# Kernel optimization log

Measured on AMD Instinct MI355X. Metric: run time of the kernel, lower is better.

The kernel has to match this reference:

```python
import jax, jax.numpy as jnp
import numpy as np

B, A, S, D, OUT = 8, 16384, 2048, 512, 512
REDUCTION = "mean"  # matches init_kwargs


def setup_inputs() -> dict:
    key = jax.random.key(0)
    k1, k2, k3 = jax.random.split(key, 3)
    input_rep = jax.random.normal(k1, (B, A, D), jnp.float32)
    # sorted residue ids per protein (atoms are stored residue-by-residue)
    aa_res_ids = jnp.sort(jax.random.randint(k2, (B, A), 0, S), axis=-1).astype(jnp.int32)
    input_aa_len = jnp.full((B,), A, jnp.int32)
    input_seq_len = jnp.full((B,), S, jnp.int32)
    W = jax.random.normal(k3, (OUT, D), jnp.float32) / np.sqrt(D)
    bias = jnp.zeros((OUT,), jnp.float32)
    return {"input_rep": input_rep, "aa_res_ids": aa_res_ids,
            "input_aa_len": input_aa_len, "input_seq_len": input_seq_len,
            "W": W, "bias": bias}


def _pool(input_rep, aa_res_ids, input_aa_len, input_seq_len):
    # input_rep: [B, A, D]; aa_res_ids: [B, A] in [0, S)
    Bv, Av, Dv = input_rep.shape
    valid = jnp.arange(Av)[None, :] < input_aa_len[:, None]          # [B, A] atoms within aa_len
    seg = jnp.arange(Bv)[:, None] * S + aa_res_ids                   # flatten (b, res_id) -> segment id
    seg = jnp.where(valid, seg, Bv * S)                              # invalid atoms -> dummy segment
    nseg = Bv * S + 1
    seg_f = seg.reshape(-1)
    counts = jax.ops.segment_sum(valid.reshape(-1).astype(input_rep.dtype), seg_f,
                                 num_segments=nseg)[: Bv * S].reshape(Bv, S)
    if REDUCTION == "mean":
        sums = jax.ops.segment_sum(input_rep.reshape(Bv * Av, Dv), seg_f,
                                   num_segments=nseg)[: Bv * S].reshape(Bv, S, Dv)
        pooled = sums / jnp.maximum(counts, 1)[..., None]
    elif REDUCTION == "max":
        vals = jnp.where(valid[..., None], input_rep, -jnp.inf).reshape(Bv * Av, Dv)
        pooled = jax.ops.segment_max(vals, seg_f, num_segments=nseg)[: Bv * S].reshape(Bv, S, Dv)
        pooled = jnp.where((counts > 0)[..., None], pooled, 0.0)
    else:
        raise ValueError("Unsupported reduction method: {}".format(REDUCTION))
    in_seq = jnp.arange(S)[None, :] < input_seq_len[:, None]         # [B, S] positions within seq_len
    filled = (counts > 0) & in_seq                                   # residues that received >=1 atom
    n_fill = filled.sum(axis=1)                                      # [B]
    avg = (pooled * filled[..., None]).sum(axis=1) / jnp.maximum(n_fill, 1)[:, None].astype(input_rep.dtype)
    # unfilled-but-in-range positions get the per-protein average of filled residues; out-of-range stay 0
    out = jnp.where(filled[..., None], pooled,
                    jnp.where(in_seq[..., None], avg[:, None, :], jnp.zeros((), input_rep.dtype)))
    return out


def reference(input_rep, aa_res_ids, input_aa_len, input_seq_len, W, bias):
    out = _pool(input_rep, aa_res_ids, input_aa_len, input_seq_len)  # [B, S, D]
    return out @ W.T + bias                                          # [B, S, OUT]
```

## Files before the change

kernel.cpp:

```cpp
#include <hip/hip_runtime.h>
#include <cstdint>
#include <cstddef>

#define Bv 8
#define Av 16384
#define Sv 2048
#define Dv 512
#define OUTv 512
#define Mv (Bv * Sv)

using u16 = unsigned short;
using f32x4 = __attribute__((ext_vector_type(4))) float;
using bf16x8 = __attribute__((ext_vector_type(8))) short;

__device__ __forceinline__ u16 f2bf(float x) {
  union { float f; uint32_t u; } v; v.f = x;
  uint32_t u = v.u;
  uint32_t r = u + 0x7FFFu + ((u >> 16) & 1u);
  return (u16)(r >> 16);
}
__device__ __forceinline__ float bf2f(u16 h) {
  union { uint32_t u; float f; } v; v.u = ((uint32_t)h) << 16; return v.f;
}

__device__ __forceinline__ void gl_lds16(const void* g, void* s) {
  __builtin_amdgcn_global_load_lds(
      (const __attribute__((address_space(1))) unsigned int*)g,
      (__attribute__((address_space(3))) unsigned int*)s, 16, 0, 0);
}

__global__ __launch_bounds__(128)
void pool_kernel(const float* __restrict__ rep, const int* __restrict__ res_ids,
                 const int* __restrict__ aa_len, u16* __restrict__ pooled,
                 int* __restrict__ counts) {
  const int bs = blockIdx.x;
  const int b = bs >> 11;
  const int s = bs & (Sv - 1);
  int alen = aa_len[b];
  alen = alen < 0 ? 0 : (alen > Av ? Av : alen);
  const int* ids = res_ids + b * Av;
  int lo = 0, hi = alen;
  while (lo < hi) { int mid = (lo + hi) >> 1; if (ids[mid] < s) lo = mid + 1; else hi = mid; }
  const int start = lo;
  hi = alen;
  while (lo < hi) { int mid = (lo + hi) >> 1; if (ids[mid] <= s) lo = mid + 1; else hi = mid; }
  const int end = lo;
  const int cnt = end - start;

  const int t = threadIdx.x;
  float a0 = 0.f, a1 = 0.f, a2 = 0.f, a3 = 0.f;
  float b0 = 0.f, b1 = 0.f, b2 = 0.f, b3 = 0.f;
  const float* base = rep + (size_t)b * Av * Dv + t * 4;
  int a = start;
  for (; a + 2 <= end; a += 2) {
    float4 v = *(const float4*)(base + (size_t)a * Dv);
    float4 w = *(const float4*)(base + (size_t)(a + 1) * Dv);
    a0 += v.x; a1 += v.y; a2 += v.z; a3 += v.w;
    b0 += w.x; b1 += w.y; b2 += w.z; b3 += w.w;
  }
  if (a < end) {
    float4 v = *(const float4*)(base + (size_t)a * Dv);
    a0 += v.x; a1 += v.y; a2 += v.z; a3 += v.w;
  }
  a0 += b0; a1 += b1; a2 += b2; a3 += b3;
  const float inv = cnt > 0 ? 1.0f / (float)cnt : 0.0f;
  ushort4 o = { f2bf(a0 * inv), f2bf(a1 * inv), f2bf(a2 * inv), f2bf(a3 * inv) };
  *(ushort4*)(pooled + (size_t)bs * Dv + t * 4) = o;
  if (t == 0) counts[bs] = cnt;
}

__global__ __launch_bounds__(256)
void wconv_kernel(const float* __restrict__ W, u16* __restrict__ Wb) {
  const int i = (blockIdx.x * 256 + threadIdx.x) * 4;
  float4 v = *(const float4*)(W + i);
  ushort4 o = { f2bf(v.x), f2bf(v.y), f2bf(v.z), f2bf(v.w) };
  *(ushort4*)(Wb + i) = o;
}

__global__ __launch_bounds__(128)
void avg_kernel(const u16* __restrict__ pooled, const int* __restrict__ counts,
                const int* __restrict__ seq_len, float* __restrict__ avg_sum,
                int* __restrict__ n_fill) {
  const int b = blockIdx.x;
  const int chunk = blockIdx.y;
  const int t = threadIdx.x;
  int slen = seq_len[b];
  slen = slen < 0 ? 0 : (slen > Sv ? Sv : slen);
  const int s0 = chunk * 128;
  float a0 = 0.f, a1 = 0.f, a2 = 0.f, a3 = 0.f;
  int filled = 0;
  for (int s = s0; s < s0 + 128; ++s) {
    if (s < slen && counts[b * Sv + s] > 0) {
      ++filled;
      ushort4 v = *(const ushort4*)(pooled + ((size_t)(b * Sv + s)) * Dv + t * 4);
      a0 += bf2f(v.x); a1 += bf2f(v.y); a2 += bf2f(v.z); a3 += bf2f(v.w);
    }
  }
  atomicAdd(&avg_sum[b * Dv + t * 4 + 0], a0);
  atomicAdd(&avg_sum[b * Dv + t * 4 + 1], a1);
  atomicAdd(&avg_sum[b * Dv + t * 4 + 2], a2);
  atomicAdd(&avg_sum[b * Dv + t * 4 + 3], a3);
  if (t == 0) atomicAdd(&n_fill[b], filled);
}

__global__ __launch_bounds__(64)
void fixup_kernel(u16* __restrict__ pooled, const int* __restrict__ counts,
                  const int* __restrict__ seq_len, const float* __restrict__ avg_sum,
                  const int* __restrict__ n_fill) {
  const int bs = blockIdx.x;
  const int b = bs >> 11;
  const int s = bs & (Sv - 1);
  int slen = seq_len[b];
  slen = slen < 0 ? 0 : (slen > Sv ? Sv : slen);
  const int cnt = counts[bs];
  const int t = threadIdx.x;
  if (s >= slen) {
    if (cnt != 0) {
      ushort4 z = {0, 0, 0, 0};
      *(ushort4*)(pooled + (size_t)bs * Dv + t * 8) = z;
      *(ushort4*)(pooled + (size_t)bs * Dv + t * 8 + 4) = z;
    }
    return;
  }
  if (cnt > 0) return;
  const int nf = n_fill[b];
  const float inv = 1.0f / (float)(nf > 0 ? nf : 1);
  float4 v0 = *(const float4*)(avg_sum + b * Dv + t * 8);
  float4 v1 = *(const float4*)(avg_sum + b * Dv + t * 8 + 4);
  ushort4 o0 = { f2bf(v0.x * inv), f2bf(v0.y * inv), f2bf(v0.z * inv), f2bf(v0.w * inv) };
  ushort4 o1 = { f2bf(v1.x * inv), f2bf(v1.y * inv), f2bf(v1.z * inv), f2bf(v1.w * inv) };
  *(ushort4*)(pooled + (size_t)bs * Dv + t * 8) = o0;
  *(ushort4*)(pooled + (size_t)bs * Dv + t * 8 + 4) = o1;
}

#define BM 128
#define BN 128
#define BK 64

__global__ __launch_bounds__(256, 2)
void gemm_kernel(const u16* __restrict__ A, const u16* __restrict__ Bw,
                 const float* __restrict__ bias, float* __restrict__ out) {
  __shared__ alignas(16) u16 As[BM * BK];
  __shared__ alignas(16) u16 Bs[BN * BK];
  const int tid = threadIdx.x;
  const int m0 = blockIdx.x * BM;
  const int n0 = blockIdx.y * BN;
  const int lane = tid & 63;
  const int wave = tid >> 6;
  const int wm = (wave & 1) * 64;
  const int wn = (wave >> 1) * 64;
  const int fr = lane & 15;
  const int fq = lane >> 4;

  f32x4 acc[4][4];
#pragma unroll
  for (int i = 0; i < 4; ++i)
#pragma unroll
    for (int j = 0; j < 4; ++j) acc[i][j] = (f32x4){0.f, 0.f, 0.f, 0.f};

  const char* Ab = (const char*)A;
  const char* Bb = (const char*)Bw;

  for (int k0 = 0; k0 < Dv; k0 += BK) {
    __syncthreads();
#pragma unroll
    for (int c = 0; c < 4; ++c) {
      const int off = (c * 256 + tid) * 16;
      const int row = off >> 7;
      const int inb = off & 127;
      gl_lds16(Ab + (size_t)(m0 + row) * (Dv * 2) + k0 * 2 + inb, (char*)As + off);
      gl_lds16(Bb + (size_t)(n0 + row) * (Dv * 2) + k0 * 2 + inb, (char*)Bs + off);
    }
    __syncthreads();

#pragma unroll
    for (int ks = 0; ks < 2; ++ks) {
      bf16x8 af[4], bfv[4];
#pragma unroll
      for (int mi = 0; mi < 4; ++mi)
        af[mi] = *(const bf16x8*)(As + (wm + mi * 16 + fr) * BK + ks * 32 + fq * 8);
#pragma unroll
      for (int ni = 0; ni < 4; ++ni)
        bfv[ni] = *(const bf16x8*)(Bs + (wn + ni * 16 + fr) * BK + ks * 32 + fq * 8);
#pragma unroll
      for (int mi = 0; mi < 4; ++mi)
#pragma unroll
        for (int ni = 0; ni < 4; ++ni)
          acc[mi][ni] = __builtin_amdgcn_mfma_f32_16x16x32_bf16(bfv[ni], af[mi], acc[mi][ni], 0, 0, 0);
    }
  }

#pragma unroll
  for (int mi = 0; mi < 4; ++mi) {
    const int row = m0 + wm + mi * 16 + fr;
#pragma unroll
    for (int ni = 0; ni < 4; ++ni) {
      const int colb = n0 + wn + ni * 16 + fq * 4;
      float4 bv = *(const float4*)(bias + colb);
      f32x4 v = acc[mi][ni];
      float4 o = { v[0] + bv.x, v[1] + bv.y, v[2] + bv.z, v[3] + bv.w };
      *(float4*)(out + (size_t)row * OUTv + colb) = o;
    }
  }
}

extern "C" void kernel_launch(void* const* d_in, const int* in_sizes, int n_in,
                              void* d_out, int out_size, void* d_ws, size_t ws_size,
                              hipStream_t stream) {
  (void)in_sizes; (void)n_in; (void)out_size; (void)ws_size;
  const float* rep     = (const float*)d_in[0];
  const int*   res_ids = (const int*)d_in[1];
  const int*   aa_len  = (const int*)d_in[2];
  const int*   seq_len = (const int*)d_in[3];
  const float* W       = (const float*)d_in[4];
  const float* bias    = (const float*)d_in[5];
  float* out = (float*)d_out;

  char* ws = (char*)d_ws;
  u16*   pooled  = (u16*)ws;
  u16*   Wb      = (u16*)(ws + 16777216);
  int*   counts  = (int*)(ws + 17301504);
  float* avg_sum = (float*)(ws + 17367040);
  int*   n_fill  = (int*)(ws + 17383424);

  hipMemsetAsync(avg_sum, 0, Bv * Dv * sizeof(float) + Bv * sizeof(int), stream);

  wconv_kernel<<<(OUTv * Dv) / (256 * 4), 256, 0, stream>>>(W, Wb);
  pool_kernel<<<Mv, 128, 0, stream>>>(rep, res_ids, aa_len, pooled, counts);
  avg_kernel<<<dim3(Bv, 16), 128, 0, stream>>>(pooled, counts, seq_len, avg_sum, n_fill);
  fixup_kernel<<<Mv, 64, 0, stream>>>(pooled, counts, seq_len, avg_sum, n_fill);
  gemm_kernel<<<dim3(Mv / BM, OUTv / BN), 256, 0, stream>>>(pooled, Wb, bias, out);
}
```

Before: 446.7 us.

## Precompute residue segment offsets, widen pool unroll, split avg over more blocks

Adds a kernel that scatters per-residue start offsets from the sorted residue ids, so each pool block reads two offsets instead of running two binary searches over global memory. The pool loop is unrolled to four independent row loads with separate accumulators to expose more memory parallelism. The average kernel is split into 128 chunks of 16 residues per protein to raise occupancy, at the cost of more atomics. This adds one extra launch, and the starts kernel's zero-length and tail-fill loops run serially in single threads.

Result: faster. 429.3 us (-3.9%).

```diff
diff --git a/kernel.cpp b/kernel.cpp
--- a/kernel.cpp
+++ b/kernel.cpp
@@ -29,44 +29,65 @@
       (__attribute__((address_space(3))) unsigned int*)s, 16, 0, 0);
 }
 
+__global__ __launch_bounds__(256)
+void starts_kernel(const int* __restrict__ res_ids, const int* __restrict__ aa_len,
+                   int* __restrict__ starts) {
+  const int b = blockIdx.y;
+  const int a = blockIdx.x * 256 + threadIdx.x;
+  int alen = aa_len[b];
+  alen = alen < 0 ? 0 : (alen > Av ? Av : alen);
+  int* st = starts + b * (Sv + 1);
+  if (a >= alen) {
+    if (a == 0) {
+      for (int s = 0; s <= Sv; ++s) st[s] = 0;
+    }
+    return;
+  }
+  const int* ids = res_ids + b * Av;
+  const int id = ids[a];
+  const int p = (a == 0) ? -1 : ids[a - 1];
+  for (int s = p + 1; s <= id; ++s) st[s] = a;
+  if (a == alen - 1) {
+    for (int s = id + 1; s <= Sv; ++s) st[s] = alen;
+  }
+}
+
 __global__ __launch_bounds__(128)
-void pool_kernel(const float* __restrict__ rep, const int* __restrict__ res_ids,
-                 const int* __restrict__ aa_len, u16* __restrict__ pooled,
-                 int* __restrict__ counts) {
+void pool_kernel(const float* __restrict__ rep, const int* __restrict__ starts,
+                 u16* __restrict__ pooled) {
   const int bs = blockIdx.x;
   const int b = bs >> 11;
   const int s = bs & (Sv - 1);
-  int alen = aa_len[b];
-  alen = alen < 0 ? 0 : (alen > Av ? Av : alen);
-  const int* ids = res_ids + b * Av;
-  int lo = 0, hi = alen;
-  while (lo < hi) { int mid = (lo + hi) >> 1; if (ids[mid] < s) lo = mid + 1; else hi = mid; }
-  const int start = lo;
-  hi = alen;
-  while (lo < hi) { int mid = (lo + hi) >> 1; if (ids[mid] <= s) lo = mid + 1; else hi = mid; }
-  const int end = lo;
+  const int* st = starts + b * (Sv + 1);
+  const int start = st[s];
+  const int end = st[s + 1];
   const int cnt = end - start;
 
   const int t = threadIdx.x;
-  float a0 = 0.f, a1 = 0.f, a2 = 0.f, a3 = 0.f;
-  float b0 = 0.f, b1 = 0.f, b2 = 0.f, b3 = 0.f;
+  float p0 = 0.f, p1 = 0.f, p2 = 0.f, p3 = 0.f;
+  float q0 = 0.f, q1 = 0.f, q2 = 0.f, q3 = 0.f;
+  float r0 = 0.f, r1 = 0.f, r2 = 0.f, r3 = 0.f;
+  float w0 = 0.f, w1 = 0.f, w2 = 0.f, w3 = 0.f;
   const float* base = rep + (size_t)b * Av * Dv + t * 4;
   int a = start;
-  for (; a + 2 <= end; a += 2) {
+  for (; a + 4 <= end; a += 4) {
+    float4 v0 = *(const float4*)(base + (size_t)(a + 0) * Dv);
+    float4 v1 = *(const float4*)(base + (size_t)(a + 1) * Dv);
+    float4 v2 = *(const float4*)(base + (size_t)(a + 2) * Dv);
+    float4 v3 = *(const float4*)(base + (size_t)(a + 3) * Dv);
+    p0 += v0.x; p1 += v0.y; p2 += v0.z; p3 += v0.w;
+    q0 += v1.x; q1 += v1.y; q2 += v1.z; q3 += v1.w;
+    r0 += v2.x; r1 += v2.y; r2 += v2.z; r3 += v2.w;
+    w0 += v3.x; w1 += v3.y; w2 += v3.z; w3 += v3.w;
+  }
+  for (; a < end; ++a) {
     float4 v = *(const float4*)(base + (size_t)a * Dv);
-    float4 w = *(const float4*)(base + (size_t)(a + 1) * Dv);
-    a0 += v.x; a1 += v.y; a2 += v.z; a3 += v.w;
-    b0 += w.x; b1 += w.y; b2 += w.z; b3 += w.w;
-  }
-  if (a < end) {
-    float4 v = *(const float4*)(base + (size_t)a * Dv);
-    a0 += v.x; a1 += v.y; a2 += v.z; a3 += v.w;
-  }
-  a0 += b0; a1 += b1; a2 += b2; a3 += b3;
+    p0 += v.x; p1 += v.y; p2 += v.z; p3 += v.w;
+  }
+  p0 += q0 + r0 + w0; p1 += q1 + r1 + w1; p2 += q2 + r2 + w2; p3 += q3 + r3 + w3;
   const float inv = cnt > 0 ? 1.0f / (float)cnt : 0.0f;
-  ushort4 o = { f2bf(a0 * inv), f2bf(a1 * inv), f2bf(a2 * inv), f2bf(a3 * inv) };
+  ushort4 o = { f2bf(p0 * inv), f2bf(p1 * inv), f2bf(p2 * inv), f2bf(p3 * inv) };
   *(ushort4*)(pooled + (size_t)bs * Dv + t * 4) = o;
-  if (t == 0) counts[bs] = cnt;
 }
 
 __global__ __launch_bounds__(256)
@@ -78,7 +99,7 @@
 }
 
 __global__ __launch_bounds__(128)
-void avg_kernel(const u16* __restrict__ pooled, const int* __restrict__ counts,
+void avg_kernel(const u16* __restrict__ pooled, const int* __restrict__ starts,
                 const int* __restrict__ seq_len, float* __restrict__ avg_sum,
                 int* __restrict__ n_fill) {
   const int b = blockIdx.x;
@@ -86,11 +107,12 @@
   const int t = threadIdx.x;
   int slen = seq_len[b];
   slen = slen < 0 ? 0 : (slen > Sv ? Sv : slen);
-  const int s0 = chunk * 128;
+  const int* st = starts + b * (Sv + 1);
+  const int s0 = chunk * 16;
   float a0 = 0.f, a1 = 0.f, a2 = 0.f, a3 = 0.f;
   int filled = 0;
-  for (int s = s0; s < s0 + 128; ++s) {
-    if (s < slen && counts[b * Sv + s] > 0) {
+  for (int s = s0; s < s0 + 16; ++s) {
+    if (s < slen && st[s + 1] - st[s] > 0) {
       ++filled;
       ushort4 v = *(const ushort4*)(pooled + ((size_t)(b * Sv + s)) * Dv + t * 4);
       a0 += bf2f(v.x); a1 += bf2f(v.y); a2 += bf2f(v.z); a3 += bf2f(v.w);
@@ -100,11 +122,11 @@
   atomicAdd(&avg_sum[b * Dv + t * 4 + 1], a1);
   atomicAdd(&avg_sum[b * Dv + t * 4 + 2], a2);
   atomicAdd(&avg_sum[b * Dv + t * 4 + 3], a3);
-  if (t == 0) atomicAdd(&n_fill[b], filled);
+  if (t == 0 && filled > 0) atomicAdd(&n_fill[b], filled);
 }
 
 __global__ __launch_bounds__(64)
-void fixup_kernel(u16* __restrict__ pooled, const int* __restrict__ counts,
+void fixup_kernel(u16* __restrict__ pooled, const int* __restrict__ starts,
                   const int* __restrict__ seq_len, const float* __restrict__ avg_sum,
                   const int* __restrict__ n_fill) {
   const int bs = blockIdx.x;
@@ -112,7 +134,8 @@
   const int s = bs & (Sv - 1);
   int slen = seq_len[b];
   slen = slen < 0 ? 0 : (slen > Sv ? Sv : slen);
-  const int cnt = counts[bs];
+  const int* st = starts + b * (Sv + 1);
+  const int cnt = st[s + 1] - st[s];
   const int t = threadIdx.x;
   if (s >= slen) {
     if (cnt != 0) {
@@ -219,15 +242,16 @@
   char* ws = (char*)d_ws;
   u16*   pooled  = (u16*)ws;
   u16*   Wb      = (u16*)(ws + 16777216);
-  int*   counts  = (int*)(ws + 17301504);
-  float* avg_sum = (float*)(ws + 17367040);
-  int*   n_fill  = (int*)(ws + 17383424);
+  int*   starts  = (int*)(ws + 17301504);
+  float* avg_sum = (float*)(ws + 17367072);
+  int*   n_fill  = (int*)(ws + 17383456);
 
   hipMemsetAsync(avg_sum, 0, Bv * Dv * sizeof(float) + Bv * sizeof(int), stream);
 
   wconv_kernel<<<(OUTv * Dv) / (256 * 4), 256, 0, stream>>>(W, Wb);
-  pool_kernel<<<Mv, 128, 0, stream>>>(rep, res_ids, aa_len, pooled, counts);
-  avg_kernel<<<dim3(Bv, 16), 128, 0, stream>>>(pooled, counts, seq_len, avg_sum, n_fill);
-  fixup_kernel<<<Mv, 64, 0, stream>>>(pooled, counts, seq_len, avg_sum, n_fill);
+  starts_kernel<<<dim3(Av / 256, Bv), 256, 0, stream>>>(res_ids, aa_len, starts);
+  pool_kernel<<<Mv, 128, 0, stream>>>(rep, starts, pooled);
+  avg_kernel<<<dim3(Bv, 128), 128, 0, stream>>>(pooled, starts, seq_len, avg_sum, n_fill);
+  fixup_kernel<<<Mv, 64, 0, stream>>>(pooled, starts, seq_len, avg_sum, n_fill);
   gemm_kernel<<<dim3(Mv / BM, OUTv / BN), 256, 0, stream>>>(pooled, Wb, bias, out);
 }
```
